# Kernel tuning notes

Measured on AMD Instinct MI355X. Metric: run time of the kernel, lower is better.

## Reference

```python
import jax, jax.numpy as jnp
import numpy as np

V, E, H, DK, L, F, NQ, C = 32000, 128, 16, 8, 4, 512, 4, 10
B, S = 8, 512
EPS = 1e-5


def _layernorm(x, g, b):
    m = jnp.mean(x, axis=-1, keepdims=True)
    v = jnp.mean((x - m) ** 2, axis=-1, keepdims=True)
    return (x - m) / jnp.sqrt(v + EPS) * g + b


def _ring_measure(c):
    # c: (..., 8) per-wire cosines cos(x_i + theta_i) after RX encode + trainable RX.
    # After CNOT(0,1)..CNOT(6,7),CNOT(7,0): <Z_i> = prod_{j<=i} c_j (i>=1), <Z_0> = prod_{j>=1} c_j.
    p = jnp.cumprod(c, axis=-1)
    z0 = jnp.prod(c[..., 1:], axis=-1, keepdims=True)
    return jnp.concatenate([z0, p[..., 1:]], axis=-1)


def _pos_encoding(seq_len, dim):
    pos = jnp.arange(seq_len, dtype=jnp.float32)[:, None]
    div = jnp.exp(jnp.arange(0, dim, 2, dtype=jnp.float32) * (-np.log(10000.0) / dim))
    pe = jnp.zeros((seq_len, dim), jnp.float32)
    pe = pe.at[:, 0::2].set(jnp.sin(pos * div))
    pe = pe.at[:, 1::2].set(jnp.cos(pos * div))
    return pe


def setup_inputs() -> dict:
    key = jax.random.key(0)
    ks = jax.random.split(key, 14)
    pi = np.pi
    return {
        "tokens": jax.random.randint(ks[0], (B, S), 0, V),
        "emb": jax.random.normal(ks[1], (V, E), jnp.float32) * 0.02,
        "attn_theta": jax.random.uniform(ks[2], (L, DK), jnp.float32, -pi, pi),
        "ffn_theta": jax.random.uniform(ks[3], (L, NQ), jnp.float32, -pi, pi),
        "Wo": jax.random.normal(ks[4], (L, E, E), jnp.float32) / np.sqrt(E),
        "W1": jax.random.normal(ks[5], (L, F, NQ), jnp.float32) / np.sqrt(NQ),
        "W2": jax.random.normal(ks[6], (L, E, F), jnp.float32) / np.sqrt(F),
        "ln1_g": jnp.ones((L, E), jnp.float32),
        "ln1_b": jnp.zeros((L, E), jnp.float32),
        "ln2_g": jnp.ones((L, E), jnp.float32),
        "ln2_b": jnp.zeros((L, E), jnp.float32),
        "Wc": jax.random.normal(ks[7], (C, E), jnp.float32) / np.sqrt(E),
        "bc": jnp.zeros((C,), jnp.float32),
    }


def reference(tokens, emb, attn_theta, ffn_theta, Wo, W1, W2,
              ln1_g, ln1_b, ln2_g, ln2_b, Wc, bc):
    b, s = tokens.shape
    h = emb[tokens] + _pos_encoding(s, E)  # (B,S,E); dropout is identity in eval
    for l in range(L):
        # --- quantum multi-head attention (q=k=v=x; shared QLayer across heads) ---
        xh = h.reshape(b, s, H, DK).transpose(0, 2, 1, 3)          # (B,H,S,DK)
        enc = _ring_measure(jnp.cos(xh + attn_theta[l]))            # (B,H,S,DK)
        scores = jnp.einsum('bhsd,bhtd->bhst', enc, enc) / np.sqrt(DK)
        attn = jax.nn.softmax(scores, axis=-1)
        o = jnp.einsum('bhst,bhtd->bhsd', attn, enc)
        o = o.transpose(0, 2, 1, 3).reshape(b, s, E) @ Wo[l].T
        h = _layernorm(h + o, ln1_g[l], ln1_b[l])
        # --- quantum feed-forward: <Z_i> = cos(x_i) * cos(theta_i), first NQ dims ---
        meas = jnp.cos(h[..., :NQ]) * jnp.cos(ffn_theta[l])          # (B,S,NQ)
        f = jax.nn.relu(meas @ W1[l].T) @ W2[l].T
        h = _layernorm(h + f, ln2_g[l], ln2_b[l])
    pooled = jnp.mean(h, axis=1)                                     # (B,E)
    return pooled @ Wc.T + bc                                        # (B,C)
```

## Files before the change

kernel.cpp:

```cpp
#include <hip/hip_runtime.h>
#include <math.h>

#define BB  8
#define SS  512
#define EE  128
#define HH  16
#define LL  4
#define FF  512
#define CC  10

typedef _Float16 h2 __attribute__((ext_vector_type(2)));
typedef _Float16 h4 __attribute__((ext_vector_type(4)));
typedef float f32x16 __attribute__((ext_vector_type(16)));

__global__ __launch_bounds__(256) void prep_kernel(
    const int* __restrict__ tokens, const float* __restrict__ emb,
    const float* __restrict__ Wo, const float* __restrict__ W2,
    float* __restrict__ h, _Float16* __restrict__ WoB, _Float16* __restrict__ W2B)
{
    int i = blockIdx.x * 256 + threadIdx.x;
    {
        int e  = i & 127;
        int bs = i >> 7;
        int s  = bs & 511;
        int tok = tokens[bs];
        int half = e >> 1;
        float ang = (float)s * expf(-0.07195578415606394f * (float)(2 * half));
        float pe  = (e & 1) ? cosf(ang) : sinf(ang);
        h[i] = emb[(size_t)tok * EE + e] + pe;
    }
    if (i < LL * 16384) {
        int jj = i & 3, lane = (i >> 2) & 63, nt = (i >> 8) & 3,
            kt = (i >> 10) & 15, l = i >> 14;
        int e = nt * 32 + (lane & 31);
        int k = kt * 8 + (lane >> 5) * 4 + jj;
        WoB[i] = (_Float16)Wo[((size_t)l * EE + e) * EE + k];
    }
    if (i < LL * 65536) {
        int jj = i & 3, lane = (i >> 2) & 63, nt = (i >> 8) & 3,
            kt = (i >> 10) & 63, l = i >> 16;
        int e = nt * 32 + (lane & 31);
        int j = kt * 8 + (lane >> 5) * 4 + jj;
        W2B[i] = (_Float16)W2[((size_t)l * EE + e) * FF + j];
    }
}

__device__ __forceinline__ void ring_from_x(
    const float4 xa, const float4 xb, const float4 tha, const float4 thb,
    float* o)
{
    float c0 = cosf(xa.x + tha.x), c1 = cosf(xa.y + tha.y),
          c2 = cosf(xa.z + tha.z), c3 = cosf(xa.w + tha.w),
          c4 = cosf(xb.x + thb.x), c5 = cosf(xb.y + thb.y),
          c6 = cosf(xb.z + thb.z), c7 = cosf(xb.w + thb.w);
    o[0] = c1 * c2 * c3 * c4 * c5 * c6 * c7;
    float cum = c0;
    cum *= c1; o[1] = cum;  cum *= c2; o[2] = cum;
    cum *= c3; o[3] = cum;  cum *= c4; o[4] = cum;
    cum *= c5; o[5] = cum;  cum *= c6; o[6] = cum;
    cum *= c7; o[7] = cum;
}

__global__ __launch_bounds__(256, 2) void attn_kernel(
    const float* __restrict__ h, const float* __restrict__ theta8,
    float* __restrict__ o)
{
    __shared__ _Float16 encA[2][SS][4];
    __shared__ _Float16 encT[9][524];
    int blk = blockIdx.x;
    int bh = blk >> 2, qpart = blk & 3;
    int b = bh >> 4, hh = bh & 15;
    int tid = threadIdx.x;

    float4 tha = ((const float4*)theta8)[0];
    float4 thb = ((const float4*)theta8)[1];

#pragma unroll
    for (int kk = 0; kk < 2; kk++) {
        int k = tid + kk * 256;
        const float* hp = h + ((size_t)(b * SS + k) * EE + hh * 8);
        float oo[8];
        ring_from_x(*(const float4*)hp, *(const float4*)(hp + 4), tha, thb, oo);
        h4 lo = {(_Float16)oo[0], (_Float16)oo[1], (_Float16)oo[2], (_Float16)oo[3]};
        h4 hi = {(_Float16)oo[4], (_Float16)oo[5], (_Float16)oo[6], (_Float16)oo[7]};
        *(h4*)&encA[0][k][0] = lo;
        *(h4*)&encA[1][k][0] = hi;
#pragma unroll
        for (int d = 0; d < 8; d++) encT[d][k] = (_Float16)oo[d];
        encT[8][k] = (_Float16)1.0f;
    }
    __syncthreads();

    int lane = tid & 63, wv = tid >> 6;
    int col = lane & 31, hf = lane >> 5;
    int qtile = qpart * 128 + wv * 32;

    h4 bq = *(const h4*)&encA[hf][qtile + col][0];

    const float SC = 0.35355339059327373f * 1.4426950408889634f;
    f32x16 Oacc = {};
    for (int kt = 0; kt < SS; kt += 32) {
        h4 ak = *(const h4*)&encA[hf][kt + col][0];
        f32x16 Cz = {};
        f32x16 C = __builtin_amdgcn_mfma_f32_32x32x8f16(ak, bq, Cz, 0, 0, 0);
        h2 ph[8];
#pragma unroll
        for (int r = 0; r < 16; r += 2) {
            float x0 = C[r] * SC, x1 = C[r + 1] * SC;
            float w0, w1;
            asm("v_exp_f32 %0, %1" : "=v"(w0) : "v"(x0));
            asm("v_exp_f32 %0, %1" : "=v"(w1) : "v"(x1));
            ph[r >> 1] = (h2)__builtin_amdgcn_cvt_pkrtz(w0, w1);
        }
#pragma unroll
        for (int j = 0; j < 4; j++) {
            h4 ap = {ph[2 * j][0], ph[2 * j][1], ph[2 * j + 1][0], ph[2 * j + 1][1]};
            h4 bv = {};
            if (col <= 8)
                bv = *(const h4*)&encT[col][kt + 8 * j + 4 * hf];
            Oacc = __builtin_amdgcn_mfma_f32_32x32x8f16(ap, bv, Oacc, 0, 0, 0);
        }
    }

#pragma unroll
    for (int r = 0; r < 16; r++) {
        float rs  = __shfl(Oacc[r], 8, 32);
        float inv = __builtin_amdgcn_rcpf(rs);
        if (col < 8) {
            int q = qtile + (r & 3) + 8 * (r >> 2) + 4 * hf;
            o[((size_t)(b * SS + q)) * EE + hh * 8 + col] = Oacc[r] * inv;
        }
    }
}

__global__ __launch_bounds__(512, 2) void fused_kernel(
    float* __restrict__ h, const float* __restrict__ o,
    const _Float16* __restrict__ WoB, const _Float16* __restrict__ W2B,
    const float* __restrict__ W1, const float* __restrict__ ffn_theta,
    const float* __restrict__ ln1g, const float* __restrict__ ln1b,
    const float* __restrict__ ln2g, const float* __restrict__ ln2b)
{
    __shared__ _Float16 oA[32][132];
    __shared__ _Float16 hid16[32][516];
    __shared__ float vL[16][128];
    __shared__ float hL[16][128];
    __shared__ __align__(16) float measL[16][4];
    __shared__ float meanL[16], rstdL[16];

    int tid = threadIdx.x;
    int t0  = blockIdx.x * 16;

    {
        int t = tid >> 5, c4 = tid & 31;
        float4 ov = ((const float4*)o)[(size_t)(t0 + t) * 32 + c4];
        h4 hv = {(_Float16)ov.x, (_Float16)ov.y, (_Float16)ov.z, (_Float16)ov.w};
        *(h4*)&oA[t][c4 * 4] = hv;
        float4 hvf = ((const float4*)h)[(size_t)(t0 + t) * 32 + c4];
        *(float4*)&hL[t][c4 * 4] = hvf;
    }
    __syncthreads();

    int lane = tid & 63, wv = tid >> 6;
    int arow = lane & 31, hf = lane >> 5;
    int col  = lane & 31;
    int nt = wv & 3, kh = wv >> 2;

    f32x16 Cw = {};
    for (int kt = kh * 8; kt < kh * 8 + 8; kt++) {
        h4 a = *(const h4*)&oA[arow][kt * 8 + hf * 4];
        h4 bfrag = *(const h4*)&WoB[((size_t)(kt * 4 + nt) * 64 + lane) * 4];
        Cw = __builtin_amdgcn_mfma_f32_32x32x8f16(a, bfrag, Cw, 0, 0, 0);
    }
    if (kh == 0) {
#pragma unroll
        for (int r = 0; r < 8; r++)
            vL[(r & 3) + 8 * (r >> 2) + 4 * hf][nt * 32 + col] = Cw[r];
    }
    __syncthreads();
    if (kh == 1) {
#pragma unroll
        for (int r = 0; r < 8; r++)
            vL[(r & 3) + 8 * (r >> 2) + 4 * hf][nt * 32 + col] += Cw[r];
    }
    __syncthreads();

    int tt = tid >> 5, l32 = tid & 31;
    {
        float sm = 0.f, sq = 0.f;
#pragma unroll
        for (int i = 0; i < 4; i++) {
            float x = vL[tt][l32 + 32 * i] + hL[tt][l32 + 32 * i];
            sm += x; sq += x * x;
        }
#pragma unroll
        for (int ofs = 16; ofs >= 1; ofs >>= 1) {
            sm += __shfl_xor(sm, ofs);
            sq += __shfl_xor(sq, ofs);
        }
        if (l32 == 0) {
            float mu = sm * (1.f / 128.f);
            meanL[tt] = mu;
            rstdL[tt] = rsqrtf(sq * (1.f / 128.f) - mu * mu + 1e-5f);
        }
    }
    __syncthreads();

    int e = tid & 127, g = tid >> 7;
    float ge1 = ln1g[e], be1 = ln1b[e];
    float h1[4];
#pragma unroll
    for (int t = 0; t < 4; t++) {
        int idx = g * 4 + t;
        float v = vL[idx][e] + hL[idx][e];
        h1[t] = (v - meanL[idx]) * rstdL[idx] * ge1 + be1;
    }
    if (e < 4) {
        float cth = cosf(ffn_theta[e]);
#pragma unroll
        for (int t = 0; t < 4; t++) measL[g * 4 + t][e] = cosf(h1[t]) * cth;
    }
    __syncthreads();

    {
        float4 w1v = ((const float4*)W1)[tid];
#pragma unroll
        for (int t = 0; t < 16; t++) {
            float4 mv = *(const float4*)&measL[t][0];
            float hv = mv.x * w1v.x + mv.y * w1v.y + mv.z * w1v.z + mv.w * w1v.w;
            hid16[t][tid] = (_Float16)fmaxf(hv, 0.f);
        }
    }
    __syncthreads();

    f32x16 Cf = {};
    for (int kt = kh * 32; kt < kh * 32 + 32; kt++) {
        h4 a = *(const h4*)&hid16[arow][kt * 8 + hf * 4];
        h4 bfrag = *(const h4*)&W2B[((size_t)(kt * 4 + nt) * 64 + lane) * 4];
        Cf = __builtin_amdgcn_mfma_f32_32x32x8f16(a, bfrag, Cf, 0, 0, 0);
    }
    if (kh == 0) {
#pragma unroll
        for (int r = 0; r < 8; r++)
            vL[(r & 3) + 8 * (r >> 2) + 4 * hf][nt * 32 + col] = Cf[r];
    }
    __syncthreads();
    if (kh == 1) {
#pragma unroll
        for (int r = 0; r < 8; r++)
            vL[(r & 3) + 8 * (r >> 2) + 4 * hf][nt * 32 + col] += Cf[r];
    }
    __syncthreads();

    float v2[4];
#pragma unroll
    for (int t = 0; t < 4; t++) {
        int idx = g * 4 + t;
        v2[t] = h1[t] + vL[idx][e];
        hL[idx][e] = v2[t];
    }
    __syncthreads();
    {
        float sm = 0.f, sq = 0.f;
#pragma unroll
        for (int i = 0; i < 4; i++) {
            float x = hL[tt][l32 + 32 * i];
            sm += x; sq += x * x;
        }
#pragma unroll
        for (int ofs = 16; ofs >= 1; ofs >>= 1) {
            sm += __shfl_xor(sm, ofs);
            sq += __shfl_xor(sq, ofs);
        }
        if (l32 == 0) {
            float mu = sm * (1.f / 128.f);
            meanL[tt] = mu;
            rstdL[tt] = rsqrtf(sq * (1.f / 128.f) - mu * mu + 1e-5f);
        }
    }
    __syncthreads();
    float ge2 = ln2g[e], be2 = ln2b[e];
#pragma unroll
    for (int t = 0; t < 4; t++) {
        int idx = g * 4 + t;
        h[(size_t)(t0 + idx) * 128 + e] = (v2[t] - meanL[idx]) * rstdL[idx] * ge2 + be2;
    }
}

__global__ __launch_bounds__(256) void head_kernel(
    const float* __restrict__ h, const float* __restrict__ Wc,
    const float* __restrict__ bc, float* __restrict__ out)
{
    __shared__ float4 red[8][32];
    __shared__ float pooled[EE];
    int b = blockIdx.x, tid = threadIdx.x;
    int eq = tid & 31, sg = tid >> 5;
    const float4* h4p = (const float4*)h + (size_t)b * SS * 32;
    float4 acc = make_float4(0, 0, 0, 0);
    for (int r = 0; r < 64; r++) {
        int s = r * 8 + sg;
        float4 x = h4p[(size_t)s * 32 + eq];
        acc.x += x.x; acc.y += x.y; acc.z += x.z; acc.w += x.w;
    }
    red[sg][eq] = acc;
    __syncthreads();
    if (sg == 0) {
        float4 a = red[0][eq];
#pragma unroll
        for (int i = 1; i < 8; i++) {
            float4 x = red[i][eq];
            a.x += x.x; a.y += x.y; a.z += x.z; a.w += x.w;
        }
        const float s = 1.f / (float)SS;
        *(float4*)&pooled[eq * 4] = make_float4(a.x * s, a.y * s, a.z * s, a.w * s);
    }
    __syncthreads();
    if (tid < 160) {
        int c = tid >> 4, l16 = tid & 15;
        float p = 0.f;
#pragma unroll
        for (int i = 0; i < 8; i++) {
            int k = l16 + i * 16;
            p += pooled[k] * Wc[(size_t)c * EE + k];
        }
#pragma unroll
        for (int ofs = 8; ofs >= 1; ofs >>= 1) p += __shfl_xor(p, ofs);
        if (l16 == 0) out[b * CC + c] = p + bc[c];
    }
}

extern "C" void kernel_launch(void* const* d_in, const int* in_sizes, int n_in,
                              void* d_out, int out_size, void* d_ws, size_t ws_size,
                              hipStream_t stream)
{
    const int*   tokens     = (const int*)d_in[0];
    const float* emb        = (const float*)d_in[1];
    const float* attn_theta = (const float*)d_in[2];
    const float* ffn_theta  = (const float*)d_in[3];
    const float* Wo         = (const float*)d_in[4];
    const float* W1         = (const float*)d_in[5];
    const float* W2         = (const float*)d_in[6];
    const float* ln1g       = (const float*)d_in[7];
    const float* ln1b       = (const float*)d_in[8];
    const float* ln2g       = (const float*)d_in[9];
    const float* ln2b       = (const float*)d_in[10];
    const float* Wc         = (const float*)d_in[11];
    const float* bc         = (const float*)d_in[12];
    float* out = (float*)d_out;

    float* ws  = (float*)d_ws;
    float* h   = ws;
    float* o   = ws + 524288;
    _Float16* WoB = (_Float16*)(ws + 1048576);
    _Float16* W2B = (_Float16*)(ws + 1081344);

    prep_kernel<<<dim3(2048), dim3(256), 0, stream>>>(tokens, emb, Wo, W2, h, WoB, W2B);

    for (int l = 0; l < LL; l++) {
        attn_kernel<<<dim3(512), dim3(256), 0, stream>>>(
            h, attn_theta + (size_t)l * 8, o);
        fused_kernel<<<dim3(256), dim3(512), 0, stream>>>(
            h, o,
            WoB + (size_t)l * 16384,
            W2B + (size_t)l * 65536,
            W1 + (size_t)l * 2048,
            ffn_theta + (size_t)l * 4,
            ln1g + (size_t)l * EE, ln1b + (size_t)l * EE,
            ln2g + (size_t)l * EE, ln2b + (size_t)l * EE);
    }

    head_kernel<<<dim3(BB), dim3(256), 0, stream>>>(h, Wc, bc, out);
}
```

Measured before the change: 101.5 us.

## Halve fused-kernel token tile, drop split-K, use hardware cosine in attention

The fused Wo/FFN kernel now handles 8 tokens per 256-thread block instead of 16 per 512-thread block, doubling the grid. Each wave now covers the full K range with two interleaved MFMA accumulators, which removes the split-K two-phase LDS reduction and its extra barriers. In the attention prologue, cosf is replaced by a v_fract plus v_cos_f32 sequence, and each thread encodes two adjacent keys so encT can take paired half2 stores. The costs are that half the MFMA M rows in the fused kernel now carry padding, weight fragments are loaded by twice as many blocks, and the hardware cosine is less accurate.

```diff
diff --git a/kernel.cpp b/kernel.cpp
--- a/kernel.cpp
+++ b/kernel.cpp
@@ -12,6 +12,15 @@
 typedef _Float16 h2 __attribute__((ext_vector_type(2)));
 typedef _Float16 h4 __attribute__((ext_vector_type(4)));
 typedef float f32x16 __attribute__((ext_vector_type(16)));
+
+__device__ __forceinline__ float fastcos(float x)
+{
+    float r = x * 0.15915494309189535f;
+    asm("v_fract_f32 %0, %1" : "=v"(r) : "v"(r));
+    float c;
+    asm("v_cos_f32 %0, %1" : "=v"(c) : "v"(r));
+    return c;
+}
 
 __global__ __launch_bounds__(256) void prep_kernel(
     const int* __restrict__ tokens, const float* __restrict__ emb,
@@ -45,14 +54,14 @@
     }
 }
 
-__device__ __forceinline__ void ring_from_x(
+__device__ __forceinline__ void ring_from_x_fast(
     const float4 xa, const float4 xb, const float4 tha, const float4 thb,
     float* o)
 {
-    float c0 = cosf(xa.x + tha.x), c1 = cosf(xa.y + tha.y),
-          c2 = cosf(xa.z + tha.z), c3 = cosf(xa.w + tha.w),
-          c4 = cosf(xb.x + thb.x), c5 = cosf(xb.y + thb.y),
-          c6 = cosf(xb.z + thb.z), c7 = cosf(xb.w + thb.w);
+    float c0 = fastcos(xa.x + tha.x), c1 = fastcos(xa.y + tha.y),
+          c2 = fastcos(xa.z + tha.z), c3 = fastcos(xa.w + tha.w),
+          c4 = fastcos(xb.x + thb.x), c5 = fastcos(xb.y + thb.y),
+          c6 = fastcos(xb.z + thb.z), c7 = fastcos(xb.w + thb.w);
     o[0] = c1 * c2 * c3 * c4 * c5 * c6 * c7;
     float cum = c0;
     cum *= c1; o[1] = cum;  cum *= c2; o[2] = cum;
@@ -75,19 +84,28 @@
     float4 tha = ((const float4*)theta8)[0];
     float4 thb = ((const float4*)theta8)[1];
 
-#pragma unroll
-    for (int kk = 0; kk < 2; kk++) {
-        int k = tid + kk * 256;
-        const float* hp = h + ((size_t)(b * SS + k) * EE + hh * 8);
-        float oo[8];
-        ring_from_x(*(const float4*)hp, *(const float4*)(hp + 4), tha, thb, oo);
-        h4 lo = {(_Float16)oo[0], (_Float16)oo[1], (_Float16)oo[2], (_Float16)oo[3]};
-        h4 hi = {(_Float16)oo[4], (_Float16)oo[5], (_Float16)oo[6], (_Float16)oo[7]};
-        *(h4*)&encA[0][k][0] = lo;
-        *(h4*)&encA[1][k][0] = hi;
-#pragma unroll
-        for (int d = 0; d < 8; d++) encT[d][k] = (_Float16)oo[d];
-        encT[8][k] = (_Float16)1.0f;
+    {
+        int k0 = 2 * tid;
+        const float* hp0 = h + ((size_t)(b * SS + k0) * EE + hh * 8);
+        const float* hp1 = hp0 + EE;
+        float o0[8], o1[8];
+        ring_from_x_fast(*(const float4*)hp0, *(const float4*)(hp0 + 4), tha, thb, o0);
+        ring_from_x_fast(*(const float4*)hp1, *(const float4*)(hp1 + 4), tha, thb, o1);
+        h4 lo0 = {(_Float16)o0[0], (_Float16)o0[1], (_Float16)o0[2], (_Float16)o0[3]};
+        h4 hi0 = {(_Float16)o0[4], (_Float16)o0[5], (_Float16)o0[6], (_Float16)o0[7]};
+        h4 lo1 = {(_Float16)o1[0], (_Float16)o1[1], (_Float16)o1[2], (_Float16)o1[3]};
+        h4 hi1 = {(_Float16)o1[4], (_Float16)o1[5], (_Float16)o1[6], (_Float16)o1[7]};
+        *(h4*)&encA[0][k0][0]     = lo0;
+        *(h4*)&encA[0][k0 + 1][0] = lo1;
+        *(h4*)&encA[1][k0][0]     = hi0;
+        *(h4*)&encA[1][k0 + 1][0] = hi1;
+#pragma unroll
+        for (int d = 0; d < 8; d++) {
+            h2 pr = {(_Float16)o0[d], (_Float16)o1[d]};
+            *(h2*)&encT[d][k0] = pr;
+        }
+        h2 one2 = {(_Float16)1.0f, (_Float16)1.0f};
+        *(h2*)&encT[8][k0] = one2;
     }
     __syncthreads();
 
@@ -133,7 +151,7 @@
     }
 }
 
-__global__ __launch_bounds__(512, 2) void fused_kernel(
+__global__ __launch_bounds__(256, 2) void fused_kernel(
     float* __restrict__ h, const float* __restrict__ o,
     const _Float16* __restrict__ WoB, const _Float16* __restrict__ W2B,
     const float* __restrict__ W1, const float* __restrict__ ffn_theta,
@@ -142,13 +160,13 @@
 {
     __shared__ _Float16 oA[32][132];
     __shared__ _Float16 hid16[32][516];
-    __shared__ float vL[16][128];
-    __shared__ float hL[16][128];
-    __shared__ __align__(16) float measL[16][4];
-    __shared__ float meanL[16], rstdL[16];
+    __shared__ float vL[8][128];
+    __shared__ float hL[8][128];
+    __shared__ __align__(16) float measL[8][4];
+    __shared__ float meanL[8], rstdL[8];
 
     int tid = threadIdx.x;
-    int t0  = blockIdx.x * 16;
+    int t0  = blockIdx.x * 8;
 
     {
         int t = tid >> 5, c4 = tid & 31;
@@ -163,25 +181,20 @@
     int lane = tid & 63, wv = tid >> 6;
     int arow = lane & 31, hf = lane >> 5;
     int col  = lane & 31;
-    int nt = wv & 3, kh = wv >> 2;
-
-    f32x16 Cw = {};
-    for (int kt = kh * 8; kt < kh * 8 + 8; kt++) {
-        h4 a = *(const h4*)&oA[arow][kt * 8 + hf * 4];
-        h4 bfrag = *(const h4*)&WoB[((size_t)(kt * 4 + nt) * 64 + lane) * 4];
-        Cw = __builtin_amdgcn_mfma_f32_32x32x8f16(a, bfrag, Cw, 0, 0, 0);
-    }
-    if (kh == 0) {
-#pragma unroll
-        for (int r = 0; r < 8; r++)
-            vL[(r & 3) + 8 * (r >> 2) + 4 * hf][nt * 32 + col] = Cw[r];
-    }
-    __syncthreads();
-    if (kh == 1) {
-#pragma unroll
-        for (int r = 0; r < 8; r++)
-            vL[(r & 3) + 8 * (r >> 2) + 4 * hf][nt * 32 + col] += Cw[r];
-    }
+    int nt = wv;
+
+    f32x16 Ca = {}, Cb = {};
+    for (int kt = 0; kt < 16; kt += 2) {
+        h4 a0 = *(const h4*)&oA[arow][kt * 8 + hf * 4];
+        h4 b0 = *(const h4*)&WoB[((size_t)((kt * 4 + nt) * 64 + lane)) * 4];
+        Ca = __builtin_amdgcn_mfma_f32_32x32x8f16(a0, b0, Ca, 0, 0, 0);
+        h4 a1 = *(const h4*)&oA[arow][(kt + 1) * 8 + hf * 4];
+        h4 b1 = *(const h4*)&WoB[((size_t)(((kt + 1) * 4 + nt) * 64 + lane)) * 4];
+        Cb = __builtin_amdgcn_mfma_f32_32x32x8f16(a1, b1, Cb, 0, 0, 0);
+    }
+#pragma unroll
+    for (int r = 0; r < 4; r++)
+        vL[r + 4 * hf][nt * 32 + col] = Ca[r] + Cb[r];
     __syncthreads();
 
     int tt = tid >> 5, l32 = tid & 31;
@@ -221,34 +234,31 @@
     }
     __syncthreads();
 
-    {
-        float4 w1v = ((const float4*)W1)[tid];
-#pragma unroll
-        for (int t = 0; t < 16; t++) {
+#pragma unroll
+    for (int jj = 0; jj < 2; jj++) {
+        int j = jj * 256 + tid;
+        float4 w1v = ((const float4*)W1)[j];
+#pragma unroll
+        for (int t = 0; t < 8; t++) {
             float4 mv = *(const float4*)&measL[t][0];
             float hv = mv.x * w1v.x + mv.y * w1v.y + mv.z * w1v.z + mv.w * w1v.w;
-            hid16[t][tid] = (_Float16)fmaxf(hv, 0.f);
-        }
-    }
-    __syncthreads();
-
-    f32x16 Cf = {};
-    for (int kt = kh * 32; kt < kh * 32 + 32; kt++) {
-        h4 a = *(const h4*)&hid16[arow][kt * 8 + hf * 4];
-        h4 bfrag = *(const h4*)&W2B[((size_t)(kt * 4 + nt) * 64 + lane) * 4];
-        Cf = __builtin_amdgcn_mfma_f32_32x32x8f16(a, bfrag, Cf, 0, 0, 0);
-    }
-    if (kh == 0) {
-#pragma unroll
-        for (int r = 0; r < 8; r++)
-            vL[(r & 3) + 8 * (r >> 2) + 4 * hf][nt * 32 + col] = Cf[r];
-    }
-    __syncthreads();
-    if (kh == 1) {
-#pragma unroll
-        for (int r = 0; r < 8; r++)
-            vL[(r & 3) + 8 * (r >> 2) + 4 * hf][nt * 32 + col] += Cf[r];
-    }
+            hid16[t][j] = (_Float16)fmaxf(hv, 0.f);
+        }
+    }
+    __syncthreads();
+
+    f32x16 Fa = {}, Fb = {};
+    for (int kt = 0; kt < 64; kt += 2) {
+        h4 a0 = *(const h4*)&hid16[arow][kt * 8 + hf * 4];
+        h4 b0 = *(const h4*)&W2B[((size_t)((kt * 4 + nt) * 64 + lane)) * 4];
+        Fa = __builtin_amdgcn_mfma_f32_32x32x8f16(a0, b0, Fa, 0, 0, 0);
+        h4 a1 = *(const h4*)&hid16[arow][(kt + 1) * 8 + hf * 4];
+        h4 b1 = *(const h4*)&W2B[((size_t)(((kt + 1) * 4 + nt) * 64 + lane)) * 4];
+        Fb = __builtin_amdgcn_mfma_f32_32x32x8f16(a1, b1, Fb, 0, 0, 0);
+    }
+#pragma unroll
+    for (int r = 0; r < 4; r++)
+        vL[r + 4 * hf][nt * 32 + col] = Fa[r] + Fb[r];
     __syncthreads();
 
     float v2[4];
@@ -358,7 +368,7 @@
     for (int l = 0; l < LL; l++) {
         attn_kernel<<<dim3(512), dim3(256), 0, stream>>>(
             h, attn_theta + (size_t)l * 8, o);
-        fused_kernel<<<dim3(256), dim3(512), 0, stream>>>(
+        fused_kernel<<<dim3(512), dim3(256), 0, stream>>>(
             h, o,
             WoB + (size_t)l * 16384,
             W2B + (size_t)l * 65536,
```

Result: slower. 108.5 us (+6.8%).

## Split attention over key halves, merge partial sums in fused kernel, fast cos

Applied to the files above, without the earlier changes.

Attention now splits the 512 keys into two halves across separate blocks, doubling the grid to 1024 blocks with half the shared memory. Each block writes unnormalized partial outputs and row sums, and the fused kernel adds the two halves and normalizes before the Wo projection. This is safe because scores are bounded and no running max is used. It also swaps cosf for a v_fract/v_cos hardware approximation and splits the W2 MFMA chain into two accumulators. The cost is extra global traffic for the partial buffers, recomputing the query encodings, and lower cosine accuracy.

```diff
diff --git a/kernel.cpp b/kernel.cpp
--- a/kernel.cpp
+++ b/kernel.cpp
@@ -12,6 +12,15 @@
 typedef _Float16 h2 __attribute__((ext_vector_type(2)));
 typedef _Float16 h4 __attribute__((ext_vector_type(4)));
 typedef float f32x16 __attribute__((ext_vector_type(16)));
+
+__device__ __forceinline__ float fastcos(float x)
+{
+    float r = x * 0.15915494309189535f;
+    asm("v_fract_f32 %0, %1" : "=v"(r) : "v"(r));
+    float c;
+    asm("v_cos_f32 %0, %1" : "=v"(c) : "v"(r));
+    return c;
+}
 
 __global__ __launch_bounds__(256) void prep_kernel(
     const int* __restrict__ tokens, const float* __restrict__ emb,
@@ -45,14 +54,14 @@
     }
 }
 
-__device__ __forceinline__ void ring_from_x(
+__device__ __forceinline__ void ring_from_x_fast(
     const float4 xa, const float4 xb, const float4 tha, const float4 thb,
     float* o)
 {
-    float c0 = cosf(xa.x + tha.x), c1 = cosf(xa.y + tha.y),
-          c2 = cosf(xa.z + tha.z), c3 = cosf(xa.w + tha.w),
-          c4 = cosf(xb.x + thb.x), c5 = cosf(xb.y + thb.y),
-          c6 = cosf(xb.z + thb.z), c7 = cosf(xb.w + thb.w);
+    float c0 = fastcos(xa.x + tha.x), c1 = fastcos(xa.y + tha.y),
+          c2 = fastcos(xa.z + tha.z), c3 = fastcos(xa.w + tha.w),
+          c4 = fastcos(xb.x + thb.x), c5 = fastcos(xb.y + thb.y),
+          c6 = fastcos(xb.z + thb.z), c7 = fastcos(xb.w + thb.w);
     o[0] = c1 * c2 * c3 * c4 * c5 * c6 * c7;
     float cum = c0;
     cum *= c1; o[1] = cum;  cum *= c2; o[2] = cum;
@@ -61,45 +70,54 @@
     cum *= c7; o[7] = cum;
 }
 
-__global__ __launch_bounds__(256, 2) void attn_kernel(
+__global__ __launch_bounds__(256, 4) void attn_kernel(
     const float* __restrict__ h, const float* __restrict__ theta8,
-    float* __restrict__ o)
-{
-    __shared__ _Float16 encA[2][SS][4];
-    __shared__ _Float16 encT[9][524];
+    float* __restrict__ a1, float* __restrict__ a2,
+    float* __restrict__ s1, float* __restrict__ s2)
+{
+    __shared__ _Float16 encA[2][256][4];
+    __shared__ _Float16 encT[9][260];
     int blk = blockIdx.x;
-    int bh = blk >> 2, qpart = blk & 3;
+    int bh = blk >> 3, qpart = (blk >> 1) & 3, kh = blk & 1;
     int b = bh >> 4, hh = bh & 15;
     int tid = threadIdx.x;
 
     float4 tha = ((const float4*)theta8)[0];
     float4 thb = ((const float4*)theta8)[1];
 
-#pragma unroll
-    for (int kk = 0; kk < 2; kk++) {
-        int k = tid + kk * 256;
+    {
+        int k = kh * 256 + tid;
         const float* hp = h + ((size_t)(b * SS + k) * EE + hh * 8);
         float oo[8];
-        ring_from_x(*(const float4*)hp, *(const float4*)(hp + 4), tha, thb, oo);
+        ring_from_x_fast(*(const float4*)hp, *(const float4*)(hp + 4), tha, thb, oo);
         h4 lo = {(_Float16)oo[0], (_Float16)oo[1], (_Float16)oo[2], (_Float16)oo[3]};
         h4 hi = {(_Float16)oo[4], (_Float16)oo[5], (_Float16)oo[6], (_Float16)oo[7]};
-        *(h4*)&encA[0][k][0] = lo;
-        *(h4*)&encA[1][k][0] = hi;
-#pragma unroll
-        for (int d = 0; d < 8; d++) encT[d][k] = (_Float16)oo[d];
-        encT[8][k] = (_Float16)1.0f;
-    }
-    __syncthreads();
+        *(h4*)&encA[0][tid][0] = lo;
+        *(h4*)&encA[1][tid][0] = hi;
+#pragma unroll
+        for (int d = 0; d < 8; d++) encT[d][tid] = (_Float16)oo[d];
+        encT[8][tid] = (_Float16)1.0f;
+    }
 
     int lane = tid & 63, wv = tid >> 6;
     int col = lane & 31, hf = lane >> 5;
     int qtile = qpart * 128 + wv * 32;
 
-    h4 bq = *(const h4*)&encA[hf][qtile + col][0];
+    h4 bq;
+    {
+        const float* hp = h + ((size_t)(b * SS + qtile + col) * EE + hh * 8);
+        float qq[8];
+        ring_from_x_fast(*(const float4*)hp, *(const float4*)(hp + 4), tha, thb, qq);
+        bq[0] = (_Float16)qq[4 * hf];
+        bq[1] = (_Float16)qq[4 * hf + 1];
+        bq[2] = (_Float16)qq[4 * hf + 2];
+        bq[3] = (_Float16)qq[4 * hf + 3];
+    }
+    __syncthreads();
 
     const float SC = 0.35355339059327373f * 1.4426950408889634f;
     f32x16 Oacc = {};
-    for (int kt = 0; kt < SS; kt += 32) {
+    for (int kt = 0; kt < 256; kt += 32) {
         h4 ak = *(const h4*)&encA[hf][kt + col][0];
         f32x16 Cz = {};
         f32x16 C = __builtin_amdgcn_mfma_f32_32x32x8f16(ak, bq, Cz, 0, 0, 0);
@@ -122,19 +140,22 @@
         }
     }
 
+    float* aP = kh ? a2 : a1;
+    float* sP = kh ? s2 : s1;
 #pragma unroll
     for (int r = 0; r < 16; r++) {
-        float rs  = __shfl(Oacc[r], 8, 32);
-        float inv = __builtin_amdgcn_rcpf(rs);
-        if (col < 8) {
-            int q = qtile + (r & 3) + 8 * (r >> 2) + 4 * hf;
-            o[((size_t)(b * SS + q)) * EE + hh * 8 + col] = Oacc[r] * inv;
-        }
+        int q = qtile + (r & 3) + 8 * (r >> 2) + 4 * hf;
+        if (col < 8)
+            aP[((size_t)(b * SS + q)) * EE + hh * 8 + col] = Oacc[r];
+        else if (col == 8)
+            sP[((size_t)(b * SS + q)) * HH + hh] = Oacc[r];
     }
 }
 
 __global__ __launch_bounds__(512, 2) void fused_kernel(
-    float* __restrict__ h, const float* __restrict__ o,
+    float* __restrict__ h,
+    const float* __restrict__ a1, const float* __restrict__ a2,
+    const float* __restrict__ s1, const float* __restrict__ s2,
     const _Float16* __restrict__ WoB, const _Float16* __restrict__ W2B,
     const float* __restrict__ W1, const float* __restrict__ ffn_theta,
     const float* __restrict__ ln1g, const float* __restrict__ ln1b,
@@ -146,14 +167,25 @@
     __shared__ float hL[16][128];
     __shared__ __align__(16) float measL[16][4];
     __shared__ float meanL[16], rstdL[16];
+    __shared__ float invL[16][16];
 
     int tid = threadIdx.x;
     int t0  = blockIdx.x * 16;
 
+    if (tid < 256) {
+        int t = tid >> 4, hh = tid & 15;
+        size_t idx = (size_t)(t0 + t) * HH + hh;
+        invL[t][hh] = 1.0f / (s1[idx] + s2[idx]);
+    }
+    __syncthreads();
+
     {
         int t = tid >> 5, c4 = tid & 31;
-        float4 ov = ((const float4*)o)[(size_t)(t0 + t) * 32 + c4];
-        h4 hv = {(_Float16)ov.x, (_Float16)ov.y, (_Float16)ov.z, (_Float16)ov.w};
+        float inv = invL[t][c4 >> 1];
+        float4 p1 = ((const float4*)a1)[(size_t)(t0 + t) * 32 + c4];
+        float4 p2 = ((const float4*)a2)[(size_t)(t0 + t) * 32 + c4];
+        h4 hv = {(_Float16)((p1.x + p2.x) * inv), (_Float16)((p1.y + p2.y) * inv),
+                 (_Float16)((p1.z + p2.z) * inv), (_Float16)((p1.w + p2.w) * inv)};
         *(h4*)&oA[t][c4 * 4] = hv;
         float4 hvf = ((const float4*)h)[(size_t)(t0 + t) * 32 + c4];
         *(float4*)&hL[t][c4 * 4] = hvf;
@@ -232,22 +264,25 @@
     }
     __syncthreads();
 
-    f32x16 Cf = {};
-    for (int kt = kh * 32; kt < kh * 32 + 32; kt++) {
-        h4 a = *(const h4*)&hid16[arow][kt * 8 + hf * 4];
-        h4 bfrag = *(const h4*)&W2B[((size_t)(kt * 4 + nt) * 64 + lane) * 4];
-        Cf = __builtin_amdgcn_mfma_f32_32x32x8f16(a, bfrag, Cf, 0, 0, 0);
+    f32x16 Cf0 = {}, Cf1 = {};
+    for (int kt = kh * 32; kt < kh * 32 + 32; kt += 2) {
+        h4 a0 = *(const h4*)&hid16[arow][kt * 8 + hf * 4];
+        h4 b0 = *(const h4*)&W2B[((size_t)(kt * 4 + nt) * 64 + lane) * 4];
+        Cf0 = __builtin_amdgcn_mfma_f32_32x32x8f16(a0, b0, Cf0, 0, 0, 0);
+        h4 a1f = *(const h4*)&hid16[arow][(kt + 1) * 8 + hf * 4];
+        h4 b1f = *(const h4*)&W2B[((size_t)((kt + 1) * 4 + nt) * 64 + lane) * 4];
+        Cf1 = __builtin_amdgcn_mfma_f32_32x32x8f16(a1f, b1f, Cf1, 0, 0, 0);
     }
     if (kh == 0) {
 #pragma unroll
         for (int r = 0; r < 8; r++)
-            vL[(r & 3) + 8 * (r >> 2) + 4 * hf][nt * 32 + col] = Cf[r];
+            vL[(r & 3) + 8 * (r >> 2) + 4 * hf][nt * 32 + col] = Cf0[r] + Cf1[r];
     }
     __syncthreads();
     if (kh == 1) {
 #pragma unroll
         for (int r = 0; r < 8; r++)
-            vL[(r & 3) + 8 * (r >> 2) + 4 * hf][nt * 32 + col] += Cf[r];
+            vL[(r & 3) + 8 * (r >> 2) + 4 * hf][nt * 32 + col] += Cf0[r] + Cf1[r];
     }
     __syncthreads();
 
@@ -349,17 +384,20 @@
 
     float* ws  = (float*)d_ws;
     float* h   = ws;
-    float* o   = ws + 524288;
-    _Float16* WoB = (_Float16*)(ws + 1048576);
-    _Float16* W2B = (_Float16*)(ws + 1081344);
+    float* a1  = ws + 524288;
+    float* a2  = ws + 1048576;
+    float* s1  = ws + 1572864;
+    float* s2  = ws + 1638400;
+    _Float16* WoB = (_Float16*)(ws + 1703936);
+    _Float16* W2B = (_Float16*)(ws + 1736704);
 
     prep_kernel<<<dim3(2048), dim3(256), 0, stream>>>(tokens, emb, Wo, W2, h, WoB, W2B);
 
     for (int l = 0; l < LL; l++) {
-        attn_kernel<<<dim3(512), dim3(256), 0, stream>>>(
-            h, attn_theta + (size_t)l * 8, o);
+        attn_kernel<<<dim3(1024), dim3(256), 0, stream>>>(
+            h, attn_theta + (size_t)l * 8, a1, a2, s1, s2);
         fused_kernel<<<dim3(256), dim3(512), 0, stream>>>(
-            h, o,
+            h, a1, a2, s1, s2,
             WoB + (size_t)l * 16384,
             W2B + (size_t)l * 65536,
             W1 + (size_t)l * 2048,
```

After: 102.4 us. No clear change (+0.9%).
